# Kernel tuning notes

Measured on AMD Instinct MI355X. Metric: run time of the kernel, lower is better.

Reference implementation:

```python
import jax, jax.numpy as jnp
import numpy as np

N_NODES = 50000
N_EDGES = 800000
IN_DIM = 64
HID_DIM = 128
OUT_DIM = 64
BN_EPS = 1e-5


def _glorot(key, shape):
    fan_in, fan_out = shape[0], shape[1]
    lim = (6.0 / (fan_in + fan_out)) ** 0.5
    return jax.random.uniform(key, shape, jnp.float32, -lim, lim)


def setup_inputs() -> dict:
    key = jax.random.key(0)
    ks = jax.random.split(key, 8)
    x = jax.random.normal(ks[0], (N_NODES, IN_DIM), jnp.float32)
    edge_index = jax.random.randint(ks[1], (2, N_EDGES), 0, N_NODES, jnp.int32)
    return {
        "x": x,
        "edge_index": edge_index,
        # SAGEConv1: lin_l (applied to aggregated neighbors, has bias), lin_r (root, no bias)
        "W1l": _glorot(ks[2], (IN_DIM, HID_DIM)),
        "b1": jnp.zeros((HID_DIM,), jnp.float32),
        "W1r": _glorot(ks[3], (IN_DIM, HID_DIM)),
        # BatchNorm1d params
        "gamma": jnp.ones((HID_DIM,), jnp.float32),
        "beta": jnp.zeros((HID_DIM,), jnp.float32),
        # SAGEConv2
        "W2l": _glorot(ks[4], (HID_DIM, OUT_DIM)),
        "b2": jnp.zeros((OUT_DIM,), jnp.float32),
        "W2r": _glorot(ks[5], (HID_DIM, OUT_DIM)),
    }


def _sage_conv(h, src, dst, Wl, b, Wr, deg_inv):
    # mean-aggregate neighbor features per destination node
    agg = jax.ops.segment_sum(h[src], dst, num_segments=N_NODES)  # [N, d]
    agg = agg * deg_inv[:, None]
    return agg @ Wl + b + h @ Wr


def reference(x, edge_index, W1l, b1, W1r, gamma, beta, W2l, b2, W2r):
    src, dst = edge_index[0], edge_index[1]
    deg = jax.ops.segment_sum(jnp.ones((N_EDGES,), jnp.float32), dst,
                              num_segments=N_NODES)
    deg_inv = jnp.where(deg > 0, 1.0 / jnp.maximum(deg, 1.0), 0.0)

    h = _sage_conv(x, src, dst, W1l, b1, W1r, deg_inv)  # [N, hid]
    # BatchNorm1d (training mode: batch stats over nodes, biased variance)
    mu = jnp.mean(h, axis=0)
    var = jnp.mean((h - mu) ** 2, axis=0)
    h = (h - mu) * jax.lax.rsqrt(var + BN_EPS) * gamma + beta
    h = jax.nn.relu(h)
    out = _sage_conv(h, src, dst, W2l, b2, W2r, deg_inv)  # [N, out]
    return out
```

## Files before the change

### kernel.cpp

```cpp
#include <hip/hip_runtime.h>

#define NN 50000
#define NE 800000
#define HID 128
#define OUTD 64
#define NBK 782
#define CAP 1408
#define TILE_E 4096
#define XB 3125
#define HB 196
#define NPART 8

typedef __attribute__((ext_vector_type(8))) short bf16x8;
typedef __attribute__((ext_vector_type(4))) float f32x4;

static __device__ __forceinline__ unsigned short f2bf(float f) {
    unsigned u = __float_as_uint(f);
    unsigned r = (u + 0x7FFFu + ((u >> 16) & 1u)) >> 16;
    return (unsigned short)r;
}
static __device__ __forceinline__ float bflo(unsigned u) { return __uint_as_float(u << 16); }
static __device__ __forceinline__ float bfhi(unsigned u) { return __uint_as_float(u & 0xffff0000u); }

#define ACC8(vv)                                            \
    acc[0] += bflo(vv.x); acc[1] += bfhi(vv.x);             \
    acc[2] += bflo(vv.y); acc[3] += bfhi(vv.y);             \
    acc[4] += bflo(vv.z); acc[5] += bfhi(vv.z);             \
    acc[6] += bflo(vv.w); acc[7] += bfhi(vv.w);

__global__ __launch_bounds__(256) void prep_bin_kernel(
    const float* __restrict__ x, unsigned short* __restrict__ xb,
    const float* __restrict__ W1l, const float* __restrict__ W1r,
    const float* __restrict__ W2l, const float* __restrict__ W2r,
    unsigned short* __restrict__ BT1, unsigned short* __restrict__ BT2,
    const int* __restrict__ src, const int* __restrict__ dst,
    int* __restrict__ gcur, unsigned* __restrict__ pairs)
{
    __shared__ int lcnt[NBK];
    __shared__ int lbase[NBK];
    int blk = blockIdx.x, tid = threadIdx.x;
    if (blk >= HB) {
        int b2 = blk - HB;
        if (b2 < XB) {
            int idx = b2 * 256 + tid;
            int n = idx >> 4, q = idx & 15;
            float4 v = ((const float4*)x)[idx];
            ushort4 o;
            o.x = f2bf(v.x); o.y = f2bf(v.y); o.z = f2bf(v.z); o.w = f2bf(v.w);
            *(ushort4*)(xb + (size_t)n * 64 + q * 4) = o;
        } else {
            int idx = (b2 - XB) * 256 + tid;
            int j = idx >> 7, k = idx & 127;
            float v1 = (k < 64) ? W1l[k * HID + j] : W1r[(k - 64) * HID + j];
            BT1[j * 128 + k] = f2bf(v1);
            float v2 = (j < 64) ? W2l[k * OUTD + j] : W2r[k * OUTD + (j - 64)];
            BT2[j * 128 + k] = f2bf(v2);
        }
        return;
    }
    int e0 = blk * TILE_E;
    for (int i = tid; i < NBK; i += 256) lcnt[i] = 0;
    __syncthreads();
    int s[16], d[16], loc[16];
#pragma unroll
    for (int i = 0; i < 16; i++) {
        int e = e0 + i * 256 + tid;
        if (e < NE) {
            s[i] = __builtin_nontemporal_load(&src[e]);
            d[i] = __builtin_nontemporal_load(&dst[e]);
            loc[i] = atomicAdd(&lcnt[d[i] >> 6], 1);
        }
    }
    __syncthreads();
    for (int b = tid; b < NBK; b += 256)
        lbase[b] = b * CAP + atomicAdd(&gcur[b], lcnt[b]);
    __syncthreads();
#pragma unroll
    for (int i = 0; i < 16; i++) {
        int e = e0 + i * 256 + tid;
        if (e < NE)
            pairs[lbase[d[i] >> 6] + loc[i]] =
                (unsigned)(((d[i] & 63) << 16) | s[i]);
    }
}

__global__ __launch_bounds__(512) void agg_conv1_kernel(
    const unsigned* __restrict__ pairs, const int* __restrict__ gcur,
    const unsigned short* __restrict__ xb, const unsigned short* __restrict__ BT,
    const float* __restrict__ bias, unsigned short* __restrict__ hpreb,
    float* __restrict__ sums_p, float* __restrict__ sumsq_p,
    unsigned short* __restrict__ permG, unsigned short* __restrict__ degG,
    unsigned short* __restrict__ startG)
{
    __shared__ int lcnt[64];
    __shared__ int startL[64];
    __shared__ int degL[64];
    __shared__ int lcur[64];
    __shared__ __align__(4) unsigned short permL[CAP];
    __shared__ __align__(16) unsigned short aggL[64][72];
    __shared__ float red_s[4][128];
    __shared__ float red_q[4][128];
    int b = blockIdx.x, tid = threadIdx.x;
    int lo = b * CAP;
    int cnt = gcur[b];
    if (tid < 64) lcnt[tid] = 0;
    __syncthreads();
    for (int i = tid; i < cnt; i += 512)
        atomicAdd(&lcnt[pairs[lo + i] >> 16], 1);
    __syncthreads();
    if (tid < 64) {
        int v = lcnt[tid];
        int s = v;
#pragma unroll
        for (int off = 1; off < 64; off <<= 1) {
            int t = __shfl_up(s, off, 64);
            if (tid >= off) s += t;
        }
        startL[tid] = s - v;
        degL[tid] = v;
        lcur[tid] = s - v;
        degG[b * 64 + tid] = (unsigned short)v;
        startG[b * 64 + tid] = (unsigned short)(s - v);
    }
    __syncthreads();
    for (int i = tid; i < cnt; i += 512) {
        unsigned p = pairs[lo + i];
        int pos = atomicAdd(&lcur[p >> 16], 1);
        permL[pos] = (unsigned short)(p & 0xffffu);
    }
    __syncthreads();
    int cu = (cnt + 1) >> 1;
    unsigned* pgb = (unsigned*)(permG + (size_t)b * CAP);
    for (int i = tid; i < cu; i += 512)
        pgb[i] = ((const unsigned*)permL)[i];
    int lane = tid & 63, w = tid >> 6;
    int g = lane >> 3;
    int q = lane & 7;
    int ln = w * 8 + g;
    const unsigned short* fbase = xb + q * 8;
    {
        int rs = startL[ln];
        int deg = degL[ln];
        float acc[8];
#pragma unroll
        for (int t = 0; t < 8; t++) acc[t] = 0.f;
        int i = 0;
        for (; i + 3 < deg; i += 4) {
            int s0 = permL[rs + i];
            int s1 = permL[rs + i + 1];
            int s2 = permL[rs + i + 2];
            int s3 = permL[rs + i + 3];
            uint4 v0 = *(const uint4*)(fbase + (size_t)s0 * 64);
            uint4 v1 = *(const uint4*)(fbase + (size_t)s1 * 64);
            uint4 v2 = *(const uint4*)(fbase + (size_t)s2 * 64);
            uint4 v3 = *(const uint4*)(fbase + (size_t)s3 * 64);
            ACC8(v0) ACC8(v1) ACC8(v2) ACC8(v3)
        }
        for (; i < deg; i++) {
            int s0 = permL[rs + i];
            uint4 v0 = *(const uint4*)(fbase + (size_t)s0 * 64);
            ACC8(v0)
        }
        float inv = (deg > 0) ? (1.0f / (float)deg) : 0.f;
        uint4 o;
        o.x = (unsigned)f2bf(acc[0] * inv) | ((unsigned)f2bf(acc[1] * inv) << 16);
        o.y = (unsigned)f2bf(acc[2] * inv) | ((unsigned)f2bf(acc[3] * inv) << 16);
        o.z = (unsigned)f2bf(acc[4] * inv) | ((unsigned)f2bf(acc[5] * inv) << 16);
        o.w = (unsigned)f2bf(acc[6] * inv) | ((unsigned)f2bf(acc[7] * inv) << 16);
        *(uint4*)&aggL[ln][q * 8] = o;
    }
    __syncthreads();
    int nl = lane & 15, ko = lane >> 4;
    int jh = w & 1, t = w >> 1;
    bf16x8 bfr[4][4];
    const unsigned short* bbase = BT + (size_t)(jh * 64 + nl) * 128 + ko * 8;
#pragma unroll
    for (int jg = 0; jg < 4; jg++)
#pragma unroll
        for (int ks = 0; ks < 4; ks++)
            bfr[jg][ks] = *(const bf16x8*)(bbase + jg * 16 * 128 + ks * 32);
    float4 bias4[4];
#pragma unroll
    for (int jg = 0; jg < 4; jg++)
        bias4[jg] = *(const float4*)(bias + jh * 64 + jg * 16 + ko * 4);
    float s_sum[16], s_sq[16];
#pragma unroll
    for (int tt = 0; tt < 16; tt++) { s_sum[tt] = 0.f; s_sq[tt] = 0.f; }
    int n_g = b * 64 + t * 16 + nl;
    if (n_g < NN) {
        bf16x8 a[4];
#pragma unroll
        for (int ks = 0; ks < 2; ks++)
            a[ks] = *(const bf16x8*)&aggL[t * 16 + nl][ks * 32 + ko * 8];
        const unsigned short* xrow = xb + (size_t)n_g * 64 + ko * 8;
#pragma unroll
        for (int ks = 2; ks < 4; ks++)
            a[ks] = *(const bf16x8*)(xrow + (ks - 2) * 32);
#pragma unroll
        for (int jg = 0; jg < 4; jg++) {
            f32x4 acc = {0.f, 0.f, 0.f, 0.f};
#pragma unroll
            for (int ks = 0; ks < 4; ks++)
                acc = __builtin_amdgcn_mfma_f32_16x16x32_bf16(bfr[jg][ks], a[ks], acc, 0, 0, 0);
            float v0 = acc[0] + bias4[jg].x;
            float v1 = acc[1] + bias4[jg].y;
            float v2 = acc[2] + bias4[jg].z;
            float v3 = acc[3] + bias4[jg].w;
            s_sum[jg * 4 + 0] += v0; s_sq[jg * 4 + 0] += v0 * v0;
            s_sum[jg * 4 + 1] += v1; s_sq[jg * 4 + 1] += v1 * v1;
            s_sum[jg * 4 + 2] += v2; s_sq[jg * 4 + 2] += v2 * v2;
            s_sum[jg * 4 + 3] += v3; s_sq[jg * 4 + 3] += v3 * v3;
            uint2 pk;
            pk.x = (unsigned)f2bf(v0) | ((unsigned)f2bf(v1) << 16);
            pk.y = (unsigned)f2bf(v2) | ((unsigned)f2bf(v3) << 16);
            *(uint2*)(hpreb + (size_t)n_g * 128 + jh * 64 + jg * 16 + ko * 4) = pk;
        }
    }
#pragma unroll
    for (int jg = 0; jg < 4; jg++) {
#pragma unroll
        for (int r = 0; r < 4; r++) {
            float v = s_sum[jg * 4 + r];
            v += __shfl_xor(v, 1, 64);
            v += __shfl_xor(v, 2, 64);
            v += __shfl_xor(v, 4, 64);
            v += __shfl_xor(v, 8, 64);
            float w2 = s_sq[jg * 4 + r];
            w2 += __shfl_xor(w2, 1, 64);
            w2 += __shfl_xor(w2, 2, 64);
            w2 += __shfl_xor(w2, 4, 64);
            w2 += __shfl_xor(w2, 8, 64);
            if (nl == 0) {
                red_s[t][jh * 64 + jg * 16 + ko * 4 + r] = v;
                red_q[t][jh * 64 + jg * 16 + ko * 4 + r] = w2;
            }
        }
    }
    __syncthreads();
    if (tid < 128) {
        float v = red_s[0][tid] + red_s[1][tid] + red_s[2][tid] + red_s[3][tid];
        atomicAdd(&sums_p[(b & (NPART - 1)) * 128 + tid], v);
    } else if (tid < 256) {
        int j = tid - 128;
        float v = red_q[0][j] + red_q[1][j] + red_q[2][j] + red_q[3][j];
        atomicAdd(&sumsq_p[(b & (NPART - 1)) * 128 + j], v);
    }
}

static __device__ __forceinline__ bf16x8 bnrelu8(uint4 v, const float* sc,
                                                 const float* sh, int j0) {
    float f[8];
    f[0] = bflo(v.x); f[1] = bfhi(v.x);
    f[2] = bflo(v.y); f[3] = bfhi(v.y);
    f[4] = bflo(v.z); f[5] = bfhi(v.z);
    f[6] = bflo(v.w); f[7] = bfhi(v.w);
#pragma unroll
    for (int t = 0; t < 8; t++) {
        float h = f[t] * sc[j0 + t] + sh[j0 + t];
        f[t] = h > 0.f ? h : 0.f;
    }
    unsigned r01 = (unsigned)f2bf(f[0]) | ((unsigned)f2bf(f[1]) << 16);
    unsigned r23 = (unsigned)f2bf(f[2]) | ((unsigned)f2bf(f[3]) << 16);
    unsigned r45 = (unsigned)f2bf(f[4]) | ((unsigned)f2bf(f[5]) << 16);
    unsigned r67 = (unsigned)f2bf(f[6]) | ((unsigned)f2bf(f[7]) << 16);
    uint4 o = make_uint4(r01, r23, r45, r67);
    return *(bf16x8*)&o;
}

__global__ __launch_bounds__(256) void conv2_kernel(
    const unsigned short* __restrict__ A, const unsigned short* __restrict__ BT,
    const float* __restrict__ bias,
    unsigned short* __restrict__ pb, float* __restrict__ outf,
    const float* __restrict__ sums_p, const float* __restrict__ sumsq_p,
    const float* __restrict__ gamma, const float* __restrict__ beta)
{
    __shared__ float sc[128], sh[128];
    int tid = threadIdx.x;
    int wid = tid >> 6, lane = tid & 63;
    int nl = lane & 15, ko = lane >> 4;
    if (tid < 128) {
        float s = 0.f, qq = 0.f;
#pragma unroll
        for (int p = 0; p < NPART; p++) {
            s  += sums_p[p * 128 + tid];
            qq += sumsq_p[p * 128 + tid];
        }
        float inv_n = 1.0f / (float)NN;
        float mu = s * inv_n;
        float var = qq * inv_n - mu * mu;
        float sf = gamma[tid] * rsqrtf(var + 1e-5f);
        sc[tid] = sf;
        sh[tid] = beta[tid] - mu * sf;
    }
    __syncthreads();
    int gw = blockIdx.x * 4 + wid;
    int jh = gw & 1;
    int tstride = (gridDim.x * 4) >> 1;
    const int tiles = NN / 16;
    bf16x8 bfr[4][4];
    const unsigned short* bbase = BT + (size_t)(jh * 64 + nl) * 128 + ko * 8;
#pragma unroll
    for (int jg = 0; jg < 4; jg++)
#pragma unroll
        for (int ks = 0; ks < 4; ks++)
            bfr[jg][ks] = *(const bf16x8*)(bbase + jg * 16 * 128 + ks * 32);
    float4 bias4[4];
#pragma unroll
    for (int jg = 0; jg < 4; jg++) {
        if (jh) bias4[jg] = *(const float4*)(bias + jg * 16 + ko * 4);
        else    bias4[jg] = make_float4(0.f, 0.f, 0.f, 0.f);
    }
    int tile = gw >> 1;
    uint4 a[4];
    if (tile < tiles) {
        const unsigned short* arow = A + (size_t)(tile * 16 + nl) * 128 + ko * 8;
#pragma unroll
        for (int ks = 0; ks < 4; ks++) a[ks] = *(const uint4*)(arow + ks * 32);
    }
    while (tile < tiles) {
        int nxt = tile + tstride;
        uint4 an[4];
        if (nxt < tiles) {
            const unsigned short* arow = A + (size_t)(nxt * 16 + nl) * 128 + ko * 8;
#pragma unroll
            for (int ks = 0; ks < 4; ks++) an[ks] = *(const uint4*)(arow + ks * 32);
        }
        bf16x8 af[4];
#pragma unroll
        for (int ks = 0; ks < 4; ks++)
            af[ks] = bnrelu8(a[ks], sc, sh, ks * 32 + ko * 8);
        int n_g = tile * 16 + nl;
#pragma unroll
        for (int jg = 0; jg < 4; jg++) {
            f32x4 acc = {0.f, 0.f, 0.f, 0.f};
#pragma unroll
            for (int ks = 0; ks < 4; ks++)
                acc = __builtin_amdgcn_mfma_f32_16x16x32_bf16(bfr[jg][ks], af[ks], acc, 0, 0, 0);
            float v0 = acc[0] + bias4[jg].x;
            float v1 = acc[1] + bias4[jg].y;
            float v2 = acc[2] + bias4[jg].z;
            float v3 = acc[3] + bias4[jg].w;
            if (jh == 0) {
                uint2 pk;
                pk.x = (unsigned)f2bf(v0) | ((unsigned)f2bf(v1) << 16);
                pk.y = (unsigned)f2bf(v2) | ((unsigned)f2bf(v3) << 16);
                *(uint2*)(pb + (size_t)n_g * 64 + jg * 16 + ko * 4) = pk;
            } else {
                float4 o = make_float4(v0, v1, v2, v3);
                *(float4*)(outf + (size_t)n_g * 64 + jg * 16 + ko * 4) = o;
            }
        }
#pragma unroll
        for (int ks = 0; ks < 4; ks++) a[ks] = an[ks];
        tile = nxt;
    }
}

__global__ __launch_bounds__(512) void agg2_kernel(
    const unsigned short* __restrict__ permG, const int* __restrict__ gcur,
    const unsigned short* __restrict__ degG, const unsigned short* __restrict__ startG,
    const unsigned short* __restrict__ pb, float* __restrict__ out)
{
    __shared__ __align__(4) unsigned short permL[CAP];
    __shared__ int startL[64];
    __shared__ int degL[64];
    int b = blockIdx.x, tid = threadIdx.x;
    int cnt = gcur[b];
    if (tid < 64) {
        startL[tid] = startG[b * 64 + tid];
        degL[tid] = degG[b * 64 + tid];
    }
    int cu = (cnt + 1) >> 1;
    const unsigned* pgb = (const unsigned*)(permG + (size_t)b * CAP);
    for (int i = tid; i < cu; i += 512)
        ((unsigned*)permL)[i] = pgb[i];
    __syncthreads();
    int lane = tid & 63, w = tid >> 6;
    int g = lane >> 3;
    int q = lane & 7;
    int ln = w * 8 + g;
    int node = b * 64 + ln;
    const unsigned short* fbase = pb + q * 8;
    int rs = startL[ln];
    int deg = degL[ln];
    float acc[8];
#pragma unroll
    for (int t = 0; t < 8; t++) acc[t] = 0.f;
    int i = 0;
    for (; i + 3 < deg; i += 4) {
        int s0 = permL[rs + i];
        int s1 = permL[rs + i + 1];
        int s2 = permL[rs + i + 2];
        int s3 = permL[rs + i + 3];
        uint4 v0 = *(const uint4*)(fbase + (size_t)s0 * 64);
        uint4 v1 = *(const uint4*)(fbase + (size_t)s1 * 64);
        uint4 v2 = *(const uint4*)(fbase + (size_t)s2 * 64);
        uint4 v3 = *(const uint4*)(fbase + (size_t)s3 * 64);
        ACC8(v0) ACC8(v1) ACC8(v2) ACC8(v3)
    }
    for (; i < deg; i++) {
        int s0 = permL[rs + i];
        uint4 v0 = *(const uint4*)(fbase + (size_t)s0 * 64);
        ACC8(v0)
    }
    if (node < NN) {
        float inv = (deg > 0) ? (1.0f / (float)deg) : 0.f;
        float4* op = (float4*)(out + (size_t)node * 64 + q * 8);
        float4 o0 = op[0], o1 = op[1];
        o0.x += acc[0] * inv; o0.y += acc[1] * inv;
        o0.z += acc[2] * inv; o0.w += acc[3] * inv;
        o1.x += acc[4] * inv; o1.y += acc[5] * inv;
        o1.z += acc[6] * inv; o1.w += acc[7] * inv;
        op[0] = o0; op[1] = o1;
    }
}

extern "C" void kernel_launch(void* const* d_in, const int* in_sizes, int n_in,
                              void* d_out, int out_size, void* d_ws, size_t ws_size,
                              hipStream_t stream) {
    const float* x     = (const float*)d_in[0];
    const int*   ei    = (const int*)d_in[1];
    const float* W1l   = (const float*)d_in[2];
    const float* b1    = (const float*)d_in[3];
    const float* W1r   = (const float*)d_in[4];
    const float* gamma = (const float*)d_in[5];
    const float* beta  = (const float*)d_in[6];
    const float* W2l   = (const float*)d_in[7];
    const float* b2    = (const float*)d_in[8];
    const float* W2r   = (const float*)d_in[9];
    float* out = (float*)d_out;

    char* wsb = (char*)d_ws;
    int*   gcur    = (int*)wsb;
    float* sums_p  = (float*)(wsb + 4096);
    float* sumsq_p = (float*)(wsb + 8192);
    unsigned* pairs = (unsigned*)(wsb + 12288);
    unsigned short* permG  = (unsigned short*)((char*)pairs + (size_t)NBK * CAP * 4);
    unsigned short* degG   = permG + (size_t)NBK * CAP;
    unsigned short* startG = degG + (size_t)NBK * 64;
    unsigned short* xb     = startG + (size_t)NBK * 64;
    unsigned short* hpreb  = xb + (size_t)NN * 64;
    unsigned short* pbuf   = hpreb + (size_t)NN * 128;
    unsigned short* BT1    = pbuf + (size_t)NN * 64;
    unsigned short* BT2    = BT1 + 128 * 128;

    const int* srcp = ei;
    const int* dstp = ei + NE;

    hipMemsetAsync(d_ws, 0, 12288, stream);

    prep_bin_kernel<<<HB + XB + 64, 256, 0, stream>>>(x, xb, W1l, W1r, W2l, W2r,
                                                      BT1, BT2, srcp, dstp, gcur, pairs);
    agg_conv1_kernel<<<NBK, 512, 0, stream>>>(pairs, gcur, xb, BT1, b1, hpreb,
                                              sums_p, sumsq_p, permG, degG, startG);
    conv2_kernel<<<512, 256, 0, stream>>>(hpreb, BT2, b2, pbuf, out,
                                          sums_p, sumsq_p, gamma, beta);
    agg2_kernel<<<NBK, 512, 0, stream>>>(permG, gcur, degG, startG, pbuf, out);
}
```

Baseline: 169.5 us.

## Split CSR build out of fused aggregation/conv1 kernel into separate kernel

Result: no change. 171.9 us (+1.4%).

```diff
diff --git a/kernel.cpp b/kernel.cpp
--- a/kernel.cpp
+++ b/kernel.cpp
@@ -84,55 +84,75 @@
     }
 }
 
-__global__ __launch_bounds__(512) void agg_conv1_kernel(
+__global__ __launch_bounds__(512) void csr_kernel(
     const unsigned* __restrict__ pairs, const int* __restrict__ gcur,
-    const unsigned short* __restrict__ xb, const unsigned short* __restrict__ BT,
-    const float* __restrict__ bias, unsigned short* __restrict__ hpreb,
-    float* __restrict__ sums_p, float* __restrict__ sumsq_p,
     unsigned short* __restrict__ permG, unsigned short* __restrict__ degG,
     unsigned short* __restrict__ startG)
 {
     __shared__ int lcnt[64];
+    __shared__ int lcur[64];
+    __shared__ __align__(16) unsigned pairsL[CAP];
+    __shared__ __align__(4) unsigned short permL[CAP];
+    int b = blockIdx.x, tid = threadIdx.x;
+    int lo = b * CAP;
+    int cnt = gcur[b];
+    if (tid < 64) lcnt[tid] = 0;
+    __syncthreads();
+    for (int i = tid; i < cnt; i += 512) {
+        unsigned p = pairs[lo + i];
+        pairsL[i] = p;
+        atomicAdd(&lcnt[p >> 16], 1);
+    }
+    __syncthreads();
+    if (tid < 64) {
+        int v = lcnt[tid];
+        int s = v;
+#pragma unroll
+        for (int off = 1; off < 64; off <<= 1) {
+            int t = __shfl_up(s, off, 64);
+            if (tid >= off) s += t;
+        }
+        lcur[tid] = s - v;
+        degG[b * 64 + tid] = (unsigned short)v;
+        startG[b * 64 + tid] = (unsigned short)(s - v);
+    }
+    __syncthreads();
+    for (int i = tid; i < cnt; i += 512) {
+        unsigned p = pairsL[i];
+        int pos = atomicAdd(&lcur[p >> 16], 1);
+        permL[pos] = (unsigned short)(p & 0xffffu);
+    }
+    __syncthreads();
+    int cu = (cnt + 1) >> 1;
+    unsigned* pgb = (unsigned*)(permG + (size_t)b * CAP);
+    for (int i = tid; i < cu; i += 512)
+        pgb[i] = ((const unsigned*)permL)[i];
+}
+
+__global__ __launch_bounds__(512) void gather_conv1_kernel(
+    const unsigned short* __restrict__ permG, const int* __restrict__ gcur,
+    const unsigned short* __restrict__ degG, const unsigned short* __restrict__ startG,
+    const unsigned short* __restrict__ xb, const unsigned short* __restrict__ BT,
+    const float* __restrict__ bias, unsigned short* __restrict__ hpreb,
+    float* __restrict__ sums_p, float* __restrict__ sumsq_p)
+{
     __shared__ int startL[64];
     __shared__ int degL[64];
-    __shared__ int lcur[64];
     __shared__ __align__(4) unsigned short permL[CAP];
     __shared__ __align__(16) unsigned short aggL[64][72];
     __shared__ float red_s[4][128];
     __shared__ float red_q[4][128];
     int b = blockIdx.x, tid = threadIdx.x;
-    int lo = b * CAP;
     int cnt = gcur[b];
-    if (tid < 64) lcnt[tid] = 0;
-    __syncthreads();
-    for (int i = tid; i < cnt; i += 512)
-        atomicAdd(&lcnt[pairs[lo + i] >> 16], 1);
-    __syncthreads();
     if (tid < 64) {
-        int v = lcnt[tid];
-        int s = v;
-#pragma unroll
-        for (int off = 1; off < 64; off <<= 1) {
-            int t = __shfl_up(s, off, 64);
-            if (tid >= off) s += t;
-        }
-        startL[tid] = s - v;
-        degL[tid] = v;
-        lcur[tid] = s - v;
-        degG[b * 64 + tid] = (unsigned short)v;
-        startG[b * 64 + tid] = (unsigned short)(s - v);
-    }
-    __syncthreads();
-    for (int i = tid; i < cnt; i += 512) {
-        unsigned p = pairs[lo + i];
-        int pos = atomicAdd(&lcur[p >> 16], 1);
-        permL[pos] = (unsigned short)(p & 0xffffu);
-    }
-    __syncthreads();
+        startL[tid] = startG[b * 64 + tid];
+        degL[tid] = degG[b * 64 + tid];
+    }
     int cu = (cnt + 1) >> 1;
-    unsigned* pgb = (unsigned*)(permG + (size_t)b * CAP);
+    const unsigned* pgb = (const unsigned*)(permG + (size_t)b * CAP);
     for (int i = tid; i < cu; i += 512)
-        pgb[i] = ((const unsigned*)permL)[i];
+        ((unsigned*)permL)[i] = pgb[i];
+    __syncthreads();
     int lane = tid & 63, w = tid >> 6;
     int g = lane >> 3;
     int q = lane & 7;
@@ -451,8 +471,9 @@
 
     prep_bin_kernel<<<HB + XB + 64, 256, 0, stream>>>(x, xb, W1l, W1r, W2l, W2r,
                                                       BT1, BT2, srcp, dstp, gcur, pairs);
-    agg_conv1_kernel<<<NBK, 512, 0, stream>>>(pairs, gcur, xb, BT1, b1, hpreb,
-                                              sums_p, sumsq_p, permG, degG, startG);
+    csr_kernel<<<NBK, 512, 0, stream>>>(pairs, gcur, permG, degG, startG);
+    gather_conv1_kernel<<<NBK, 512, 0, stream>>>(permG, gcur, degG, startG, xb, BT1,
+                                                 b1, hpreb, sums_p, sumsq_p);
     conv2_kernel<<<512, 256, 0, stream>>>(hpreb, BT2, b2, pbuf, out,
                                           sums_p, sumsq_p, gamma, beta);
     agg2_kernel<<<NBK, 512, 0, stream>>>(permG, gcur, degG, startG, pbuf, out);
```
